# Performance work log

Hardware: AMD Instinct MI355X
Metric: run time of the kernel (lower is better)

Reference implementation:

```python
import jax, jax.numpy as jnp
import numpy as np
from jax import lax

# Hyperparameters (match init_kwargs)
A = 0.9          # dynamic model: x_t = A * x_{t-1} + SIGMA * eps
SIGMA = 1.0
OBS_SIGMA = 1.0
LR = 0.1
ALPHA = 0.9
ITERATIONS = 3
EPS = 1e-8


def _pairwise_sq(x):
    # (B,N,N) squared euclidean distances ||x_i - x_j||^2
    x2 = jnp.sum(x * x, -1)
    sq = x2[:, :, None] + x2[:, None, :] - 2.0 * jnp.einsum('bid,bjd->bij', x, x)
    return jnp.maximum(sq, 0.0)


def _log_dynamic(x, prev):
    # logd[b,i,j] = log N(x_i ; A*prev_j, SIGMA^2 I)
    D = x.shape[-1]
    x2 = jnp.sum(x * x, -1)
    p2 = jnp.sum(prev * prev, -1)
    sq = x2[:, :, None] - 2.0 * A * jnp.einsum('bid,bjd->bij', x, prev) + (A * A) * p2[:, None, :]
    return -0.5 * sq / (SIGMA ** 2) - 0.5 * D * jnp.log(2.0 * jnp.pi * SIGMA ** 2)


def _post_grad(x, prev, obs):
    # softmax over j == max-subtract / exp / weighted-mean of d_log_dynamic in the original
    w = jax.nn.softmax(_log_dynamic(x, prev), axis=-1)                 # (B,N,N)
    mean_prev = jnp.einsum('bij,bjd->bid', w, prev)                    # sum_j w_ij * prev_j
    dyn_grad = -(x - A * mean_prev) / (SIGMA ** 2)                     # = sum_j w_ij * d_log_dynamic
    obs_grad = -(x - obs[:, None, :]) / (OBS_SIGMA ** 2)               # observation_model.d_score
    return dyn_grad + obs_grad


def _svgd(x, grad_fn):
    B, N, D = x.shape
    logN = jnp.log(jnp.asarray(N, x.dtype))
    step = jnp.zeros_like(x)
    for _ in range(ITERATIONS):
        sq = _pairwise_sq(x)                                           # (B,N,N)
        flat = jnp.sqrt(sq).reshape(B, N * N)
        med = jnp.sort(flat, axis=-1)[:, (N * N - 1) // 2]             # torch lower median of cdist
        h = (med * med / logN)[:, None, None]                          # (B,1,1) bandwidth
        rbf = jnp.exp(-sq / h)                                         # exp(-(1/h)*||x_i-x_j||^2)
        g = grad_fn(x)                                                 # (B,N,D) posterior score at particles
        kxy = jnp.einsum('bij,bjd->bid', rbf, g)                       # sum_j rbf_ij * g_j
        # sum_j d_rbf_ij = (2/h) * (x_i * sum_j rbf_ij - sum_j rbf_ij * x_j)   (avoids (B,N,N,D))
        rep = (2.0 / h) * (x * jnp.sum(rbf, -1)[..., None] - jnp.einsum('bij,bjd->bid', rbf, x))
        stein = (kxy + rep) / N
        step = ALPHA * step + (1.0 - ALPHA) * stein * stein            # RMSprop accumulator
        x = x + LR * stein / (jnp.sqrt(step) + EPS)
    return x


def setup_inputs() -> dict:
    key = jax.random.key(0)
    k1, k2, k3 = jax.random.split(key, 3)
    B, N, D = 8, 2048, 4
    return {
        'prev_state': jax.random.normal(k1, (B, N, D), jnp.float32),
        'observation': jax.random.normal(k2, (B, D), jnp.float32),
        'noise': jax.random.normal(k3, (B, N, D), jnp.float32),
    }


def reference(prev_state, observation, noise):
    N = prev_state.shape[1]
    logN = jnp.log(jnp.asarray(N, prev_state.dtype))
    # dynamic_model.sample
    state = A * prev_state + SIGMA * noise
    # post: logsumexp over i (dim=-2) of log_dynamic[b,i,j]
    log_post = jax.nn.logsumexp(_log_dynamic(state, prev_state), axis=1)   # (B,N)
    new_state = lax.stop_gradient(_svgd(state, lambda x: _post_grad(x, prev_state, observation)))
    log_weight = log_post - lax.stop_gradient(log_post) - logN             # value == -log N
    return jnp.concatenate([new_state, log_weight[..., None]], axis=-1)    # (B,N,D+1)
```

## Files before the change

### kernel.cpp

```cpp
#include <hip/hip_runtime.h>
#include <math.h>


#define NPART 2048
#define KRANK 2097151
#define LOGN_F 7.6246189861593985f
#define A_C 0.9f

__global__ __launch_bounds__(256) void k_init(const float* __restrict__ prev,
                                              const float* __restrict__ noise,
                                              float* __restrict__ x0,
                                              float* __restrict__ stepb,
                                              float* __restrict__ apb,
                                              int* __restrict__ hists) {
  int idx = blockIdx.x * 256 + threadIdx.x;
  float4 p  = ((const float4*)prev)[idx];
  float4 nz = ((const float4*)noise)[idx];
  float4 ap = make_float4(A_C*p.x, A_C*p.y, A_C*p.z, A_C*p.w);
  float4 x  = make_float4(ap.x+nz.x, ap.y+nz.y, ap.z+nz.z, ap.w+nz.w);
  ((float4*)x0)[idx]    = x;
  ((float4*)stepb)[idx] = make_float4(0.f, 0.f, 0.f, 0.f);
  ((float4*)apb)[idx]   = ap;
  ((int4*)hists)[idx] = make_int4(0, 0, 0, 0);
}

template <int PHASE>
__global__ __launch_bounds__(256) void k_hist(const float* __restrict__ x,
                                              const int* __restrict__ state,
                                              int* __restrict__ hist) {
  int b    = blockIdx.x >> 6;
  int tile = blockIdx.x & 63;
  int itile = tile & 7;
  int ktile = tile >> 3;
  __shared__ float4 sx[NPART];
  __shared__ int    sh[4096];
  for (int t = threadIdx.x; t < NPART; t += 256)
    sx[t] = ((const float4*)x)[b*NPART + t];
  for (int t = threadIdx.x; t < 4096; t += 256) sh[t] = 0;
  int sel0 = (PHASE == 1) ? state[b*4 + 0] : 0;
  __syncthreads();

  int i = itile*256 + threadIdx.x;
  float4 xi = sx[i];
  int k0 = ktile*128 + 1;
#pragma unroll 4
  for (int kk = 0; kk < 128; ++kk) {
    int k = k0 + kk;
    int j = (i + k) & (NPART - 1);
    float4 xj = sx[j];
    float dx = xi.x - xj.x, dy = xi.y - xj.y;
    float dz = xi.z - xj.z, dw = xi.w - xj.w;
    float sq = dx*dx + dy*dy + dz*dz + dw*dw;
    unsigned bits = __float_as_uint(sq);
    bool ok = (k != 1024) || (i < 1024);
    if (PHASE == 0) {
      if (ok) atomicAdd(&sh[bits >> 20], 2);
    } else {
      if (ok && (int)(bits >> 20) == sel0) atomicAdd(&sh[(bits >> 8) & 4095], 2);
    }
  }
  __syncthreads();
  for (int t = threadIdx.x; t < 4096; t += 256) {
    int c = sh[t];
    if (c) atomicAdd(&hist[b*4096 + t], c);
  }
}

__global__ __launch_bounds__(256) void k_scan0(const int* __restrict__ hist0,
                                               int* __restrict__ state) {
  int b = blockIdx.x;
  __shared__ int part[256];
  int s = 0;
  for (int c = 0; c < 16; ++c) s += hist0[b*4096 + threadIdx.x*16 + c];
  if (threadIdx.x == 0) s += NPART;
  part[threadIdx.x] = s;
  __syncthreads();
  if (threadIdx.x == 0) {
    int r = KRANK, cum = 0, ch = 0;
    for (; ch < 256; ++ch) { if (cum + part[ch] > r) break; cum += part[ch]; }
    int bin = ch * 16;
    for (;; ++bin) {
      int c = hist0[b*4096 + bin] + ((bin == 0) ? NPART : 0);
      if (cum + c > r) break;
      cum += c;
    }
    state[b*4 + 0] = bin;
    state[b*4 + 2] = r - cum;
  }
}

__global__ __launch_bounds__(256) void k_scan1(int* __restrict__ hist0,
                                               int* __restrict__ hist1,
                                               const int* __restrict__ state,
                                               float* __restrict__ hpar) {
  int b = blockIdx.x;
  __shared__ int part[256];
  int sel0 = state[b*4 + 0];
  int s = 0;
  for (int c = 0; c < 16; ++c) s += hist1[b*4096 + threadIdx.x*16 + c];
  if (threadIdx.x == 0 && sel0 == 0) s += NPART;
  part[threadIdx.x] = s;
  __syncthreads();
  if (threadIdx.x == 0) {
    int r = state[b*4 + 2], cum = 0, ch = 0;
    for (; ch < 256; ++ch) { if (cum + part[ch] > r) break; cum += part[ch]; }
    int bin = ch * 16;
    for (;; ++bin) {
      int c = hist1[b*4096 + bin] + ((sel0 == 0 && bin == 0) ? NPART : 0);
      if (cum + c > r) break;
      cum += c;
    }
    unsigned bits = (((unsigned)sel0) << 20) | (((unsigned)bin) << 8) | 128u;
    float med = sqrtf(__uint_as_float(bits));
    float h = med * med / LOGN_F;
    hpar[b*4 + 0] = h;
    hpar[b*4 + 1] = -1.0f / h;
    hpar[b*4 + 2] = 2.0f / h;
  }
  __syncthreads();
  for (int t = threadIdx.x; t < 4096; t += 256) {
    hist0[b*4096 + t] = 0;
    hist1[b*4096 + t] = 0;
  }
}

__global__ __launch_bounds__(256) void k_grad(const float* __restrict__ x,
                                              const float* __restrict__ apb,
                                              const float* __restrict__ obs,
                                              float* __restrict__ g) {
  int b = blockIdx.x >> 6;
  int iblk = blockIdx.x & 63;
  __shared__ float4 sap[NPART];
  for (int t = threadIdx.x; t < NPART; t += 256)
    sap[t] = ((const float4*)apb)[b*NPART + t];
  __syncthreads();
  int sub = threadIdx.x & 7;
  int ii  = threadIdx.x >> 3;
  int i = iblk*32 + ii;
  float4 xi = ((const float4*)x)[b*NPART + i];

  float sum = 0.f;
  float4 acc = make_float4(0.f, 0.f, 0.f, 0.f);
#pragma unroll 4
  for (int c = 0; c < 256; ++c) {
    int j = sub + 8*c;
    float4 ap = sap[j];
    float dx = xi.x - ap.x, dy = xi.y - ap.y;
    float dz = xi.z - ap.z, dw = xi.w - ap.w;
    float e = __expf(-0.5f*(dx*dx + dy*dy + dz*dz + dw*dw));
    sum += e;
    acc.x += e*ap.x; acc.y += e*ap.y; acc.z += e*ap.z; acc.w += e*ap.w;
  }
#pragma unroll
  for (int d = 1; d < 8; d <<= 1) {
    sum   += __shfl_xor(sum, d);
    acc.x += __shfl_xor(acc.x, d);
    acc.y += __shfl_xor(acc.y, d);
    acc.z += __shfl_xor(acc.z, d);
    acc.w += __shfl_xor(acc.w, d);
  }
  if (sub == 0) {
    float inv = 1.0f / sum;
    float4 ob = ((const float4*)obs)[b];
    float4 gg;
    gg.x = acc.x*inv + ob.x - 2.0f*xi.x;
    gg.y = acc.y*inv + ob.y - 2.0f*xi.y;
    gg.z = acc.z*inv + ob.z - 2.0f*xi.z;
    gg.w = acc.w*inv + ob.w - 2.0f*xi.w;
    ((float4*)g)[b*NPART + i] = gg;
  }
}

__global__ __launch_bounds__(256) void k_stein(const float* __restrict__ x,
                                               const float* __restrict__ g,
                                               const float* __restrict__ hpar,
                                               float* __restrict__ stepb,
                                               float* __restrict__ xout) {
  int b = blockIdx.x >> 6;
  int iblk = blockIdx.x & 63;
  __shared__ float4 sx[NPART];
  __shared__ float4 sg[NPART];
  for (int t = threadIdx.x; t < NPART; t += 256) {
    sx[t] = ((const float4*)x)[b*NPART + t];
    sg[t] = ((const float4*)g)[b*NPART + t];
  }
  __syncthreads();
  float neginvh = hpar[b*4 + 1];
  float two_h   = hpar[b*4 + 2];
  int sub = threadIdx.x & 7;
  int ii  = threadIdx.x >> 3;
  int i = iblk*32 + ii;
  float4 xi = sx[i];

  float S0 = 0.f;
  float4 Sx = make_float4(0.f,0.f,0.f,0.f);
  float4 Sg = make_float4(0.f,0.f,0.f,0.f);
#pragma unroll 4
  for (int c = 0; c < 256; ++c) {
    int j = sub + 8*c;
    float4 xj = sx[j];
    float4 gj = sg[j];
    float dx = xi.x - xj.x, dy = xi.y - xj.y;
    float dz = xi.z - xj.z, dw = xi.w - xj.w;
    float sq = dx*dx + dy*dy + dz*dz + dw*dw;
    float e = __expf(sq * neginvh);
    S0 += e;
    Sx.x += e*xj.x; Sx.y += e*xj.y; Sx.z += e*xj.z; Sx.w += e*xj.w;
    Sg.x += e*gj.x; Sg.y += e*gj.y; Sg.z += e*gj.z; Sg.w += e*gj.w;
  }
#pragma unroll
  for (int d = 1; d < 8; d <<= 1) {
    S0   += __shfl_xor(S0, d);
    Sx.x += __shfl_xor(Sx.x, d); Sx.y += __shfl_xor(Sx.y, d);
    Sx.z += __shfl_xor(Sx.z, d); Sx.w += __shfl_xor(Sx.w, d);
    Sg.x += __shfl_xor(Sg.x, d); Sg.y += __shfl_xor(Sg.y, d);
    Sg.z += __shfl_xor(Sg.z, d); Sg.w += __shfl_xor(Sg.w, d);
  }
  if (sub == 0) {
    const float invN = 1.0f / 2048.0f;
    float4 stein;
    stein.x = (Sg.x + two_h*(xi.x*S0 - Sx.x)) * invN;
    stein.y = (Sg.y + two_h*(xi.y*S0 - Sx.y)) * invN;
    stein.z = (Sg.z + two_h*(xi.z*S0 - Sx.z)) * invN;
    stein.w = (Sg.w + two_h*(xi.w*S0 - Sx.w)) * invN;
    float4 st = ((float4*)stepb)[b*NPART + i];
    st.x = 0.9f*st.x + 0.1f*stein.x*stein.x;
    st.y = 0.9f*st.y + 0.1f*stein.y*stein.y;
    st.z = 0.9f*st.z + 0.1f*stein.z*stein.z;
    st.w = 0.9f*st.w + 0.1f*stein.w*stein.w;
    ((float4*)stepb)[b*NPART + i] = st;
    float4 xn;
    xn.x = xi.x + 0.1f*stein.x / (sqrtf(st.x) + 1e-8f);
    xn.y = xi.y + 0.1f*stein.y / (sqrtf(st.y) + 1e-8f);
    xn.z = xi.z + 0.1f*stein.z / (sqrtf(st.z) + 1e-8f);
    xn.w = xi.w + 0.1f*stein.w / (sqrtf(st.w) + 1e-8f);
    ((float4*)xout)[b*NPART + i] = xn;
  }
}

__global__ __launch_bounds__(256) void k_out(const float* __restrict__ x,
                                             float* __restrict__ out) {
  int idx = blockIdx.x * 256 + threadIdx.x;
  float4 v = ((const float4*)x)[idx];
  float* o = out + (size_t)idx * 5;
  o[0] = v.x; o[1] = v.y; o[2] = v.z; o[3] = v.w;
  o[4] = -LOGN_F;
}

extern "C" void kernel_launch(void* const* d_in, const int* in_sizes, int n_in,
                              void* d_out, int out_size, void* d_ws, size_t ws_size,
                              hipStream_t stream) {
  const float* prev  = (const float*)d_in[0];
  const float* obs   = (const float*)d_in[1];
  const float* noise = (const float*)d_in[2];
  float* out = (float*)d_out;

  float* ws = (float*)d_ws;
  float* xA    = ws;
  float* xB    = xA + 65536;
  float* gbuf  = xB + 65536;
  float* stepb = gbuf + 65536;
  float* apb   = stepb + 65536;
  float* hpar  = apb + 65536;
  int*   state = (int*)(hpar + 32);
  int*   hist0 = state + 32;
  int*   hist1 = hist0 + 8*4096;

  k_init<<<64, 256, 0, stream>>>(prev, noise, xA, stepb, apb, hist0);

  float* xc = xA;
  float* xn = xB;
  for (int it = 0; it < 3; ++it) {
    k_hist<0><<<512, 256, 0, stream>>>(xc, state, hist0);
    k_scan0<<<8, 256, 0, stream>>>(hist0, state);
    k_hist<1><<<512, 256, 0, stream>>>(xc, state, hist1);
    k_scan1<<<8, 256, 0, stream>>>(hist0, hist1, state, hpar);
    k_grad<<<512, 256, 0, stream>>>(xc, apb, obs, gbuf);
    k_stein<<<512, 256, 0, stream>>>(xc, gbuf, hpar, stepb, xn);
    float* t = xc; xc = xn; xn = t;
  }
  k_out<<<64, 256, 0, stream>>>(xc, out);
}
```

Baseline: 340.8 us.

## Fuse median scans into histogram kernels and drop LDS staging

Each histogram pass now ends with a last-block-done scan, using an atomic counter and a threadfence, so the separate scan kernels disappear. The output write moves into the final stein kernel, and the first stein iteration skips reading step state. The grad, hist and stein kernels now read particles straight from global memory (L1/L2) instead of staging them in LDS, and use twice as many blocks with 16 lanes per particle. The repulsive term is computed from e*dx directly rather than through xi*S0 - Sx. This cuts launch count and LDS fill overhead, but makes the inner loops depend on cache hit rates for global loads.

Result: slower. 737.2 us (+116.3%).

```diff
diff --git a/kernel.cpp b/kernel.cpp
--- a/kernel.cpp
+++ b/kernel.cpp
@@ -10,44 +10,45 @@
 __global__ __launch_bounds__(256) void k_init(const float* __restrict__ prev,
                                               const float* __restrict__ noise,
                                               float* __restrict__ x0,
-                                              float* __restrict__ stepb,
                                               float* __restrict__ apb,
-                                              int* __restrict__ hists) {
+                                              int* __restrict__ hists,
+                                              int* __restrict__ ctrs) {
   int idx = blockIdx.x * 256 + threadIdx.x;
   float4 p  = ((const float4*)prev)[idx];
   float4 nz = ((const float4*)noise)[idx];
   float4 ap = make_float4(A_C*p.x, A_C*p.y, A_C*p.z, A_C*p.w);
   float4 x  = make_float4(ap.x+nz.x, ap.y+nz.y, ap.z+nz.z, ap.w+nz.w);
-  ((float4*)x0)[idx]    = x;
-  ((float4*)stepb)[idx] = make_float4(0.f, 0.f, 0.f, 0.f);
-  ((float4*)apb)[idx]   = ap;
+  ((float4*)x0)[idx]  = x;
+  ((float4*)apb)[idx] = ap;
   ((int4*)hists)[idx] = make_int4(0, 0, 0, 0);
+  if (idx < 64) ctrs[idx] = 0;
 }
 
 template <int PHASE>
 __global__ __launch_bounds__(256) void k_hist(const float* __restrict__ x,
-                                              const int* __restrict__ state,
-                                              int* __restrict__ hist) {
-  int b    = blockIdx.x >> 6;
-  int tile = blockIdx.x & 63;
-  int itile = tile & 7;
-  int ktile = tile >> 3;
-  __shared__ float4 sx[NPART];
-  __shared__ int    sh[4096];
-  for (int t = threadIdx.x; t < NPART; t += 256)
-    sx[t] = ((const float4*)x)[b*NPART + t];
+                                              int* __restrict__ state,
+                                              int* __restrict__ hist,
+                                              int* __restrict__ ctr,
+                                              float* __restrict__ hpar) {
+  int b    = blockIdx.x >> 7;
+  int sub  = blockIdx.x & 127;
+  int itile = sub >> 4;
+  int ktile = sub & 15;
+  __shared__ int sh[4096];
+  __shared__ int lastflag;
   for (int t = threadIdx.x; t < 4096; t += 256) sh[t] = 0;
   int sel0 = (PHASE == 1) ? state[b*4 + 0] : 0;
   __syncthreads();
 
   int i = itile*256 + threadIdx.x;
-  float4 xi = sx[i];
-  int k0 = ktile*128 + 1;
-#pragma unroll 4
-  for (int kk = 0; kk < 128; ++kk) {
+  const float4* xb = (const float4*)x + b*NPART;
+  float4 xi = xb[i];
+  int k0 = ktile*64 + 1;
+#pragma unroll 8
+  for (int kk = 0; kk < 64; ++kk) {
     int k = k0 + kk;
     int j = (i + k) & (NPART - 1);
-    float4 xj = sx[j];
+    float4 xj = xb[j];
     float dx = xi.x - xj.x, dy = xi.y - xj.y;
     float dz = xi.z - xj.z, dw = xi.w - xj.w;
     float sq = dx*dx + dy*dy + dz*dz + dw*dw;
@@ -60,91 +61,72 @@
     }
   }
   __syncthreads();
+  int* hb = hist + b*4096;
   for (int t = threadIdx.x; t < 4096; t += 256) {
     int c = sh[t];
-    if (c) atomicAdd(&hist[b*4096 + t], c);
-  }
-}
-
-__global__ __launch_bounds__(256) void k_scan0(const int* __restrict__ hist0,
-                                               int* __restrict__ state) {
-  int b = blockIdx.x;
+    if (c) atomicAdd(&hb[t], c);
+  }
+  __threadfence();
+  if (threadIdx.x == 0) {
+    int old = atomicAdd(&ctr[b], 1);
+    lastflag = (old == 127);
+  }
+  __syncthreads();
+  if (!lastflag) return;
+  __threadfence();
+
   __shared__ int part[256];
   int s = 0;
-  for (int c = 0; c < 16; ++c) s += hist0[b*4096 + threadIdx.x*16 + c];
-  if (threadIdx.x == 0) s += NPART;
+  for (int c = 0; c < 16; ++c)
+    s += __hip_atomic_load(&hb[threadIdx.x*16 + c], __ATOMIC_RELAXED,
+                           __HIP_MEMORY_SCOPE_AGENT);
+  if (threadIdx.x == 0 && (PHASE == 0 || sel0 == 0)) s += NPART;
   part[threadIdx.x] = s;
   __syncthreads();
   if (threadIdx.x == 0) {
-    int r = KRANK, cum = 0, ch = 0;
+    int r = (PHASE == 0) ? KRANK : state[b*4 + 2];
+    int cum = 0, ch = 0;
     for (; ch < 256; ++ch) { if (cum + part[ch] > r) break; cum += part[ch]; }
     int bin = ch * 16;
     for (;; ++bin) {
-      int c = hist0[b*4096 + bin] + ((bin == 0) ? NPART : 0);
+      int c = __hip_atomic_load(&hb[bin], __ATOMIC_RELAXED,
+                                __HIP_MEMORY_SCOPE_AGENT)
+              + ((bin == 0 && (PHASE == 0 || sel0 == 0)) ? NPART : 0);
       if (cum + c > r) break;
       cum += c;
     }
-    state[b*4 + 0] = bin;
-    state[b*4 + 2] = r - cum;
-  }
-}
-
-__global__ __launch_bounds__(256) void k_scan1(int* __restrict__ hist0,
-                                               int* __restrict__ hist1,
-                                               const int* __restrict__ state,
-                                               float* __restrict__ hpar) {
-  int b = blockIdx.x;
-  __shared__ int part[256];
-  int sel0 = state[b*4 + 0];
-  int s = 0;
-  for (int c = 0; c < 16; ++c) s += hist1[b*4096 + threadIdx.x*16 + c];
-  if (threadIdx.x == 0 && sel0 == 0) s += NPART;
-  part[threadIdx.x] = s;
-  __syncthreads();
-  if (threadIdx.x == 0) {
-    int r = state[b*4 + 2], cum = 0, ch = 0;
-    for (; ch < 256; ++ch) { if (cum + part[ch] > r) break; cum += part[ch]; }
-    int bin = ch * 16;
-    for (;; ++bin) {
-      int c = hist1[b*4096 + bin] + ((sel0 == 0 && bin == 0) ? NPART : 0);
-      if (cum + c > r) break;
-      cum += c;
-    }
-    unsigned bits = (((unsigned)sel0) << 20) | (((unsigned)bin) << 8) | 128u;
-    float med = sqrtf(__uint_as_float(bits));
-    float h = med * med / LOGN_F;
-    hpar[b*4 + 0] = h;
-    hpar[b*4 + 1] = -1.0f / h;
-    hpar[b*4 + 2] = 2.0f / h;
-  }
-  __syncthreads();
-  for (int t = threadIdx.x; t < 4096; t += 256) {
-    hist0[b*4096 + t] = 0;
-    hist1[b*4096 + t] = 0;
-  }
+    if (PHASE == 0) {
+      state[b*4 + 0] = bin;
+      state[b*4 + 2] = r - cum;
+    } else {
+      unsigned mb = (((unsigned)sel0) << 20) | (((unsigned)bin) << 8) | 128u;
+      float med = sqrtf(__uint_as_float(mb));
+      float h = med * med / LOGN_F;
+      hpar[b*4 + 1] = -1.0f / h;
+      hpar[b*4 + 2] = 2.0f / h;
+    }
+  }
+  __syncthreads();
+  for (int t = threadIdx.x; t < 4096; t += 256) hb[t] = 0;
 }
 
 __global__ __launch_bounds__(256) void k_grad(const float* __restrict__ x,
                                               const float* __restrict__ apb,
                                               const float* __restrict__ obs,
                                               float* __restrict__ g) {
-  int b = blockIdx.x >> 6;
-  int iblk = blockIdx.x & 63;
-  __shared__ float4 sap[NPART];
-  for (int t = threadIdx.x; t < NPART; t += 256)
-    sap[t] = ((const float4*)apb)[b*NPART + t];
-  __syncthreads();
-  int sub = threadIdx.x & 7;
-  int ii  = threadIdx.x >> 3;
-  int i = iblk*32 + ii;
+  int b   = blockIdx.x >> 7;
+  int ip  = threadIdx.x >> 4;
+  int sub = threadIdx.x & 15;
+  int i = (blockIdx.x & 127)*16 + ip;
+  const float4* ab = (const float4*)apb + b*NPART;
   float4 xi = ((const float4*)x)[b*NPART + i];
 
   float sum = 0.f;
   float4 acc = make_float4(0.f, 0.f, 0.f, 0.f);
-#pragma unroll 4
-  for (int c = 0; c < 256; ++c) {
-    int j = sub + 8*c;
-    float4 ap = sap[j];
+#pragma unroll 8
+  for (int c = 0; c < 128; ++c) {
+    int j = sub + 16*c;
+    float4 ap = ab[j];
     float dx = xi.x - ap.x, dy = xi.y - ap.y;
     float dz = xi.z - ap.z, dw = xi.w - ap.w;
     float e = __expf(-0.5f*(dx*dx + dy*dy + dz*dz + dw*dw));
@@ -152,7 +134,7 @@
     acc.x += e*ap.x; acc.y += e*ap.y; acc.z += e*ap.z; acc.w += e*ap.w;
   }
 #pragma unroll
-  for (int d = 1; d < 8; d <<= 1) {
+  for (int d = 1; d < 16; d <<= 1) {
     sum   += __shfl_xor(sum, d);
     acc.x += __shfl_xor(acc.x, d);
     acc.y += __shfl_xor(acc.y, d);
@@ -171,80 +153,76 @@
   }
 }
 
+template <int MODE>
 __global__ __launch_bounds__(256) void k_stein(const float* __restrict__ x,
                                                const float* __restrict__ g,
                                                const float* __restrict__ hpar,
                                                float* __restrict__ stepb,
-                                               float* __restrict__ xout) {
-  int b = blockIdx.x >> 6;
-  int iblk = blockIdx.x & 63;
-  __shared__ float4 sx[NPART];
-  __shared__ float4 sg[NPART];
-  for (int t = threadIdx.x; t < NPART; t += 256) {
-    sx[t] = ((const float4*)x)[b*NPART + t];
-    sg[t] = ((const float4*)g)[b*NPART + t];
-  }
-  __syncthreads();
+                                               float* __restrict__ xout,
+                                               float* __restrict__ outp) {
+  int b   = blockIdx.x >> 7;
+  int ip  = threadIdx.x >> 4;
+  int sub = threadIdx.x & 15;
+  int i = (blockIdx.x & 127)*16 + ip;
+  const float4* xb = (const float4*)x + b*NPART;
+  const float4* gb = (const float4*)g + b*NPART;
   float neginvh = hpar[b*4 + 1];
   float two_h   = hpar[b*4 + 2];
-  int sub = threadIdx.x & 7;
-  int ii  = threadIdx.x >> 3;
-  int i = iblk*32 + ii;
-  float4 xi = sx[i];
-
-  float S0 = 0.f;
-  float4 Sx = make_float4(0.f,0.f,0.f,0.f);
+  float4 xi = xb[i];
+
+  float4 Sd = make_float4(0.f,0.f,0.f,0.f);
   float4 Sg = make_float4(0.f,0.f,0.f,0.f);
-#pragma unroll 4
-  for (int c = 0; c < 256; ++c) {
-    int j = sub + 8*c;
-    float4 xj = sx[j];
-    float4 gj = sg[j];
+#pragma unroll 8
+  for (int c = 0; c < 128; ++c) {
+    int j = sub + 16*c;
+    float4 xj = xb[j];
+    float4 gj = gb[j];
     float dx = xi.x - xj.x, dy = xi.y - xj.y;
     float dz = xi.z - xj.z, dw = xi.w - xj.w;
     float sq = dx*dx + dy*dy + dz*dz + dw*dw;
     float e = __expf(sq * neginvh);
-    S0 += e;
-    Sx.x += e*xj.x; Sx.y += e*xj.y; Sx.z += e*xj.z; Sx.w += e*xj.w;
+    Sd.x += e*dx; Sd.y += e*dy; Sd.z += e*dz; Sd.w += e*dw;
     Sg.x += e*gj.x; Sg.y += e*gj.y; Sg.z += e*gj.z; Sg.w += e*gj.w;
   }
 #pragma unroll
-  for (int d = 1; d < 8; d <<= 1) {
-    S0   += __shfl_xor(S0, d);
-    Sx.x += __shfl_xor(Sx.x, d); Sx.y += __shfl_xor(Sx.y, d);
-    Sx.z += __shfl_xor(Sx.z, d); Sx.w += __shfl_xor(Sx.w, d);
+  for (int d = 1; d < 16; d <<= 1) {
+    Sd.x += __shfl_xor(Sd.x, d); Sd.y += __shfl_xor(Sd.y, d);
+    Sd.z += __shfl_xor(Sd.z, d); Sd.w += __shfl_xor(Sd.w, d);
     Sg.x += __shfl_xor(Sg.x, d); Sg.y += __shfl_xor(Sg.y, d);
     Sg.z += __shfl_xor(Sg.z, d); Sg.w += __shfl_xor(Sg.w, d);
   }
   if (sub == 0) {
     const float invN = 1.0f / 2048.0f;
-    float4 stein;
-    stein.x = (Sg.x + two_h*(xi.x*S0 - Sx.x)) * invN;
-    stein.y = (Sg.y + two_h*(xi.y*S0 - Sx.y)) * invN;
-    stein.z = (Sg.z + two_h*(xi.z*S0 - Sx.z)) * invN;
-    stein.w = (Sg.w + two_h*(xi.w*S0 - Sx.w)) * invN;
-    float4 st = ((float4*)stepb)[b*NPART + i];
-    st.x = 0.9f*st.x + 0.1f*stein.x*stein.x;
-    st.y = 0.9f*st.y + 0.1f*stein.y*stein.y;
-    st.z = 0.9f*st.z + 0.1f*stein.z*stein.z;
-    st.w = 0.9f*st.w + 0.1f*stein.w*stein.w;
-    ((float4*)stepb)[b*NPART + i] = st;
+    float4 sv;
+    sv.x = (Sg.x + two_h*Sd.x) * invN;
+    sv.y = (Sg.y + two_h*Sd.y) * invN;
+    sv.z = (Sg.z + two_h*Sd.z) * invN;
+    sv.w = (Sg.w + two_h*Sd.w) * invN;
+    float4 st;
+    if (MODE == 0) {
+      st = make_float4(0.1f*sv.x*sv.x, 0.1f*sv.y*sv.y,
+                       0.1f*sv.z*sv.z, 0.1f*sv.w*sv.w);
+    } else {
+      st = ((float4*)stepb)[b*NPART + i];
+      st.x = 0.9f*st.x + 0.1f*sv.x*sv.x;
+      st.y = 0.9f*st.y + 0.1f*sv.y*sv.y;
+      st.z = 0.9f*st.z + 0.1f*sv.z*sv.z;
+      st.w = 0.9f*st.w + 0.1f*sv.w*sv.w;
+    }
     float4 xn;
-    xn.x = xi.x + 0.1f*stein.x / (sqrtf(st.x) + 1e-8f);
-    xn.y = xi.y + 0.1f*stein.y / (sqrtf(st.y) + 1e-8f);
-    xn.z = xi.z + 0.1f*stein.z / (sqrtf(st.z) + 1e-8f);
-    xn.w = xi.w + 0.1f*stein.w / (sqrtf(st.w) + 1e-8f);
-    ((float4*)xout)[b*NPART + i] = xn;
-  }
-}
-
-__global__ __launch_bounds__(256) void k_out(const float* __restrict__ x,
-                                             float* __restrict__ out) {
-  int idx = blockIdx.x * 256 + threadIdx.x;
-  float4 v = ((const float4*)x)[idx];
-  float* o = out + (size_t)idx * 5;
-  o[0] = v.x; o[1] = v.y; o[2] = v.z; o[3] = v.w;
-  o[4] = -LOGN_F;
+    xn.x = xi.x + 0.1f*sv.x / (sqrtf(st.x) + 1e-8f);
+    xn.y = xi.y + 0.1f*sv.y / (sqrtf(st.y) + 1e-8f);
+    xn.z = xi.z + 0.1f*sv.z / (sqrtf(st.z) + 1e-8f);
+    xn.w = xi.w + 0.1f*sv.w / (sqrtf(st.w) + 1e-8f);
+    if (MODE != 2) {
+      ((float4*)stepb)[b*NPART + i] = st;
+      ((float4*)xout)[b*NPART + i] = xn;
+    } else {
+      float* o = outp + (size_t)(b*NPART + i) * 5;
+      o[0] = xn.x; o[1] = xn.y; o[2] = xn.z; o[3] = xn.w;
+      o[4] = -LOGN_F;
+    }
+  }
 }
 
 extern "C" void kernel_launch(void* const* d_in, const int* in_sizes, int n_in,
@@ -265,19 +243,23 @@
   int*   state = (int*)(hpar + 32);
   int*   hist0 = state + 32;
   int*   hist1 = hist0 + 8*4096;
-
-  k_init<<<64, 256, 0, stream>>>(prev, noise, xA, stepb, apb, hist0);
+  int*   ctrs  = hist1 + 8*4096;
+
+  k_init<<<64, 256, 0, stream>>>(prev, noise, xA, apb, hist0, ctrs);
 
   float* xc = xA;
   float* xn = xB;
   for (int it = 0; it < 3; ++it) {
-    k_hist<0><<<512, 256, 0, stream>>>(xc, state, hist0);
-    k_scan0<<<8, 256, 0, stream>>>(hist0, state);
-    k_hist<1><<<512, 256, 0, stream>>>(xc, state, hist1);
-    k_scan1<<<8, 256, 0, stream>>>(hist0, hist1, state, hpar);
-    k_grad<<<512, 256, 0, stream>>>(xc, apb, obs, gbuf);
-    k_stein<<<512, 256, 0, stream>>>(xc, gbuf, hpar, stepb, xn);
+    k_grad<<<1024, 256, 0, stream>>>(xc, apb, obs, gbuf);
+    k_hist<0><<<1024, 256, 0, stream>>>(xc, state, hist0, ctrs + it*16,     hpar);
+    k_hist<1><<<1024, 256, 0, stream>>>(xc, state, hist1, ctrs + it*16 + 8, hpar);
+    if (it == 0) {
+      k_stein<0><<<1024, 256, 0, stream>>>(xc, gbuf, hpar, stepb, xn, nullptr);
+    } else if (it == 1) {
+      k_stein<1><<<1024, 256, 0, stream>>>(xc, gbuf, hpar, stepb, xn, nullptr);
+    } else {
+      k_stein<2><<<1024, 256, 0, stream>>>(xc, gbuf, hpar, stepb, nullptr, out);
+    }
     float* t = xc; xc = xn; xn = t;
   }
-  k_out<<<64, 256, 0, stream>>>(xc, out);
-}
+}
```
